# Kernel tuning notes

Measured on AMD Instinct MI355X. Metric: run time of the kernel, lower is better.

The kernel has to match this reference:

```python
import jax, jax.numpy as jnp
import numpy as np

T, H = 4096, 2048

def _glorot(key, shape):
    return jax.random.uniform(key, shape, minval=-1.0, maxval=1.0) * jnp.sqrt(2.0 / sum(shape))

def setup_inputs() -> dict:
    key = jax.random.key(0)
    k_x, k_a, k_b = jax.random.split(key, 3)
    x_seq = jax.random.normal(k_x, (T, H), dtype=jnp.float32)
    a_diag = _glorot(k_a, (H,)).astype(jnp.float32)        # (H,)
    b_mat = _glorot(k_b, (H, H)).astype(jnp.float32)       # (H, H)
    return {"x_seq": x_seq, "a_diag": a_diag, "b_mat": b_mat}

def _power_kernel(a_diag, length):
    # kernel[h, k] = a_diag[h] ** k for k in [0, length).
    # Computed via cumprod (identical math to jnp.power with integer exponents,
    # but well-defined for negative a_diag and differentiable).
    h = a_diag.shape[0]
    ones = jnp.ones((h, 1), dtype=a_diag.dtype)
    pows = jnp.cumprod(jnp.broadcast_to(a_diag[:, None], (h, length - 1)), axis=1)
    return jnp.concatenate([ones, pows], axis=1)[:, None, :]  # (H, 1, T)

def reference(x_seq, a_diag, b_mat):
    seq_len, hidden_size = x_seq.shape
    s = b_mat.T @ x_seq.T                                  # (H, T)
    s_padded = jnp.pad(s, ((0, 0), (seq_len - 1, 0)))[None, :, :]  # (1, H, 2T-1)
    kernel = _power_kernel(a_diag, seq_len)                # (H, 1, T)
    kernel_flipped = jnp.flip(kernel, axis=-1)
    conv_out = jax.lax.conv_general_dilated(
        s_padded, kernel_flipped,
        window_strides=(1,), padding="VALID",
        dimension_numbers=("NCT", "OIT", "NCT"),
        feature_group_count=hidden_size,
    )                                                      # (1, H, T)
    return conv_out[0].T                                   # (T, H)
```

## Files before the change

### kernel.cpp

```cpp
#include <hip/hip_runtime.h>
#include <cstdint>
#include <cstddef>

typedef short bf16x8 __attribute__((ext_vector_type(8)));
typedef float f32x4 __attribute__((ext_vector_type(4)));

__device__ __forceinline__ unsigned short f2bf(float f) {
    union { float f; uint32_t u; } v; v.f = f;
    uint32_t r = v.u + 0x7FFFu + ((v.u >> 16) & 1u);
    return (unsigned short)(r >> 16);
}

__device__ __forceinline__ float bf2f(unsigned short u) {
    union { uint32_t u; float f; } v; v.u = (uint32_t)u << 16;
    return v.f;
}


__global__ void prep_kernel(const float* __restrict__ X,
                            unsigned short* __restrict__ Xbf, int n4,
                            const float* __restrict__ B,
                            unsigned short* __restrict__ Bt, int H,
                            int castBlocks) {
    if ((int)blockIdx.x < castBlocks) {
        int i = blockIdx.x * 256 + threadIdx.x;
        if (i < n4) {
            float4 v = ((const float4*)X)[i];
            ushort4 o;
            o.x = f2bf(v.x); o.y = f2bf(v.y); o.z = f2bf(v.z); o.w = f2bf(v.w);
            ((ushort4*)Xbf)[i] = o;
        }
        return;
    }
    __shared__ float tile[32][33];
    int tb = blockIdx.x - castBlocks;
    int tilesPerRow = H / 32;
    int bx = (tb % tilesPerRow) * 32;
    int by = (tb / tilesPerRow) * 32;
    int tx = threadIdx.x & 31, ty = threadIdx.x >> 5;
#pragma unroll
    for (int i = 0; i < 32; i += 8)
        tile[ty + i][tx] = B[(size_t)(by + ty + i) * H + bx + tx];
    __syncthreads();
#pragma unroll
    for (int i = 0; i < 32; i += 8)
        Bt[(size_t)(bx + ty + i) * H + by + tx] = f2bf(tile[tx][ty + i]);
}


__global__ __launch_bounds__(256, 2) void gemm_scan_fused(
    const unsigned short* __restrict__ A,
    const unsigned short* __restrict__ Bt,
    const float* __restrict__ Ad,
    float* __restrict__ out,
    int M, int N, int K, int gridMt)
{
    extern __shared__ char smem[];

    const int tid  = threadIdx.x;
    const int wave = tid >> 6;
    const int lane = tid & 63;

    int b = blockIdx.x;
    int mt, nt;
    if ((gridMt & 7) == 0) {
        int x = b & 7, g = b >> 3;
        int mPerX = gridMt >> 3;
        mt = x * mPerX + (g % mPerX);
        nt = g / mPerX;
    } else {
        mt = b % gridMt;
        nt = b / gridMt;
    }
    const int m0 = mt * 128;
    const int n0 = nt * 128;

    const int wm = wave >> 1;
    const int wn = wave & 1;
    const int srow = lane >> 3;
    const int scol = ((lane & 7) ^ srow) * 8;
    const int quad = lane >> 4;
    const int l16  = lane & 15;
    const int s7   = l16 & 7;
    const int koff0 = (quad ^ s7) * 16;
    const int koff1 = ((quad + 4) ^ s7) * 16;
    const int hi8  = l16 >> 3;

    f32x4 acc[4][4];
#pragma unroll
    for (int i = 0; i < 4; ++i)
#pragma unroll
        for (int j = 0; j < 4; ++j)
            acc[i][j] = (f32x4){0.f, 0.f, 0.f, 0.f};
    f32x4 wacc[2];
    wacc[0] = (f32x4){0.f, 0.f, 0.f, 0.f};
    wacc[1] = (f32x4){0.f, 0.f, 0.f, 0.f};

    const int NT = K >> 6;

    auto STAGE = [&](int bufoff, int k0) {
#pragma unroll
        for (int i = 0; i < 9; ++i) {
            const int t = wave + i * 4;
            if (t < 33) {
                const unsigned short* g;
                if (t < 17) {
                    int gr = m0 - 8 + t * 8 + srow;
                    if (gr < 0) gr = 0;
                    g = A + (size_t)gr * K + (k0 + scol);
                } else {
                    const int gr = n0 + (t - 17) * 8 + srow;
                    g = Bt + (size_t)gr * K + (k0 + scol);
                }
                __builtin_amdgcn_global_load_lds(
                    (const __attribute__((address_space(1))) void*)g,
                    (__attribute__((address_space(3))) void*)
                        (smem + bufoff + t * 1024 + lane * 16),
                    16, 0, 0);
            }
        }
    };

    STAGE(0, 0);
    __syncthreads();

    for (int t = 0; t < NT; ++t) {
        const int cur = (t & 1) * 33792;
        if (t + 1 < NT)
            STAGE((~t & 1) * 33792, (t + 1) * 64);

        const char* base = smem + cur;
#pragma unroll
        for (int kk = 0; kk < 2; ++kk) {
            const int co = kk ? koff1 : koff0;
            bf16x8 af[4], bfr[4], aw, bw0, bw1;
            aw = *(const bf16x8*)(base + hi8 * 1024 + s7 * 128 + co);
#pragma unroll
            for (int im = 0; im < 4; ++im)
                af[im] = *(const bf16x8*)(base +
                    (1 + wm * 8 + im * 2 + hi8) * 1024 + s7 * 128 + co);
#pragma unroll
            for (int in = 0; in < 4; ++in)
                bfr[in] = *(const bf16x8*)(base +
                    (17 + wn * 8 + in * 2 + hi8) * 1024 + s7 * 128 + co);
            bw0 = *(const bf16x8*)(base +
                    (17 + (wave * 2 + 0) * 2 + hi8) * 1024 + s7 * 128 + co);
            bw1 = *(const bf16x8*)(base +
                    (17 + (wave * 2 + 1) * 2 + hi8) * 1024 + s7 * 128 + co);
            wacc[0] = __builtin_amdgcn_mfma_f32_16x16x32_bf16(aw, bw0, wacc[0], 0, 0, 0);
            wacc[1] = __builtin_amdgcn_mfma_f32_16x16x32_bf16(aw, bw1, wacc[1], 0, 0, 0);
#pragma unroll
            for (int im = 0; im < 4; ++im)
#pragma unroll
                for (int in = 0; in < 4; ++in)
                    acc[im][in] = __builtin_amdgcn_mfma_f32_16x16x32_bf16(
                        af[im], bfr[in], acc[im][in], 0, 0, 0);
        }
        __syncthreads();
    }

    unsigned short* Sl = (unsigned short*)smem;
#pragma unroll
    for (int im = 0; im < 4; ++im)
#pragma unroll
        for (int in = 0; in < 4; ++in) {
            const int col = wn * 64 + in * 16 + l16;
#pragma unroll
            for (int r = 0; r < 4; ++r) {
                const int row = 8 + wm * 64 + im * 16 + quad * 4 + r;
                Sl[row * 132 + col] = f2bf(acc[im][in][r]);
            }
        }
    if (quad < 2) {
#pragma unroll
        for (int j = 0; j < 2; ++j) {
            const int wcol = (wave * 2 + j) * 16 + l16;
#pragma unroll
            for (int r = 0; r < 4; ++r)
                Sl[(quad * 4 + r) * 132 + wcol] = f2bf(wacc[j][r]);
        }
    }
    __syncthreads();

    const int c = tid & 127;
    const int q = tid >> 7;
    const float aa = Ad[n0 + c];
    float y = 0.f;
    if (mt != 0 || q != 0) {
#pragma unroll
        for (int i = 0; i < 8; ++i)
            y = fmaf(aa, y, bf2f(Sl[(q * 64 + i) * 132 + c]));
    }
    const size_t ob = (size_t)(m0 + q * 64) * N + n0 + c;
    const unsigned short* Sr = Sl + (8 + q * 64) * 132 + c;
    for (int t = 0; t < 64; ++t) {
        y = fmaf(aa, y, bf2f(Sr[t * 132]));
        out[ob + (size_t)t * N] = y;
    }
}


__global__ __launch_bounds__(256, 2) void gemm_sk_bf16out(
    const unsigned short* __restrict__ A,
    const unsigned short* __restrict__ Bt,
    unsigned short* __restrict__ S0, unsigned short* __restrict__ S1,
    int M, int N, int K, int gridM, int gridN)
{
    __shared__ __attribute__((aligned(16))) unsigned short sA[256 * 64];
    __shared__ __attribute__((aligned(16))) unsigned short sB[128 * 64];

    const int tid  = threadIdx.x;
    const int wave = tid >> 6;
    const int lane = tid & 63;

    int b = blockIdx.x;
    int mt, nt, kt;
    if ((gridM & 7) == 0) {
        int x = b & 7, g = b >> 3;
        int mPerX = gridM >> 3;
        int ml = g % mPerX, g2 = g / mPerX;
        nt = g2 % gridN;
        kt = g2 / gridN;
        mt = x * mPerX + ml;
    } else {
        mt = b % gridM;
        nt = (b / gridM) % gridN;
        kt = b / (gridM * gridN);
    }
    const int m0 = mt * 256;
    const int n0 = nt * 128;
    const int ksize = K / 2;
    const int kbase = kt * ksize;

    const int srow = lane >> 3;
    const int scol = ((lane & 7) ^ srow) * 8;

    const int quad = lane >> 4;
    const int l16  = lane & 15;
    const int wm = wave >> 1;
    const int wn = wave & 1;
    const int s7 = l16 & 7;
    const int c0 = (quad ^ s7) * 16;
    const int c1 = ((quad + 4) ^ s7) * 16;

    f32x4 acc[8][4];
#pragma unroll
    for (int i = 0; i < 8; ++i)
#pragma unroll
        for (int j = 0; j < 4; ++j)
            acc[i][j] = (f32x4){0.f, 0.f, 0.f, 0.f};

    const unsigned short* Ab = A  + (size_t)m0 * K;
    const unsigned short* Bb = Bt + (size_t)n0 * K;

    const int rA = (wm * 16 + (l16 >> 3)) * 1024 + s7 * 128;
    const int rB = (wn * 8  + (l16 >> 3)) * 1024 + s7 * 128;

    for (int k0 = kbase; k0 < kbase + ksize; k0 += 64) {
#pragma unroll
        for (int i = 0; i < 8; ++i) {
            const int t = wave * 8 + i;
            const unsigned short* ga = Ab + (size_t)(t * 8 + srow) * K + (k0 + scol);
            __builtin_amdgcn_global_load_lds(
                (const __attribute__((address_space(1))) void*)ga,
                (__attribute__((address_space(3))) void*)(sA + t * 512),
                16, 0, 0);
        }
#pragma unroll
        for (int i = 0; i < 4; ++i) {
            const int t = wave * 4 + i;
            const unsigned short* gb = Bb + (size_t)(t * 8 + srow) * K + (k0 + scol);
            __builtin_amdgcn_global_load_lds(
                (const __attribute__((address_space(1))) void*)gb,
                (__attribute__((address_space(3))) void*)(sB + t * 512),
                16, 0, 0);
        }
        __syncthreads();

#pragma unroll
        for (int kk = 0; kk < 2; ++kk) {
            const int co = kk ? c1 : c0;
            bf16x8 af[8], bfr[4];
#pragma unroll
            for (int im = 0; im < 8; ++im)
                af[im] = *(const bf16x8*)((const char*)sA + rA + im * 2048 + co);
#pragma unroll
            for (int in = 0; in < 4; ++in)
                bfr[in] = *(const bf16x8*)((const char*)sB + rB + in * 2048 + co);
#pragma unroll
            for (int im = 0; im < 8; ++im)
#pragma unroll
                for (int in = 0; in < 4; ++in)
                    acc[im][in] = __builtin_amdgcn_mfma_f32_16x16x32_bf16(
                        af[im], bfr[in], acc[im][in], 0, 0, 0);
        }
        __syncthreads();
    }

    unsigned short* __restrict__ S = (kt == 0) ? S0 : S1;
#pragma unroll
    for (int im = 0; im < 8; ++im) {
#pragma unroll
        for (int in = 0; in < 4; ++in) {
            int col = n0 + wn * 64 + in * 16 + l16;
#pragma unroll
            for (int r = 0; r < 4; ++r) {
                int row = m0 + wm * 128 + im * 16 + quad * 4 + r;
                S[(size_t)row * N + col] = f2bf(acc[im][in][r]);
            }
        }
    }
}


__device__ __forceinline__ void stage_tile128(
    const unsigned short* __restrict__ Ab, const unsigned short* __restrict__ Bb,
    unsigned short* sAp, unsigned short* sBp,
    int wave, int srow, int scol, int k0, int K)
{
#pragma unroll
    for (int i = 0; i < 4; ++i) {
        const int t = wave * 4 + i;
        const unsigned short* ga = Ab + (size_t)(t * 8 + srow) * K + (k0 + scol);
        __builtin_amdgcn_global_load_lds(
            (const __attribute__((address_space(1))) void*)ga,
            (__attribute__((address_space(3))) void*)(sAp + t * 512),
            16, 0, 0);
        const unsigned short* gb = Bb + (size_t)(t * 8 + srow) * K + (k0 + scol);
        __builtin_amdgcn_global_load_lds(
            (const __attribute__((address_space(1))) void*)gb,
            (__attribute__((address_space(3))) void*)(sBp + t * 512),
            16, 0, 0);
    }
}

__global__ __launch_bounds__(256, 4) void gemm_f32out(
    const unsigned short* __restrict__ A,
    const unsigned short* __restrict__ Bt,
    float* __restrict__ C, int M, int N, int K, int gridM)
{
    __shared__ __attribute__((aligned(16))) unsigned short sA[128 * 64];
    __shared__ __attribute__((aligned(16))) unsigned short sB[128 * 64];

    const int tid  = threadIdx.x;
    const int wave = tid >> 6;
    const int lane = tid & 63;

    int b = blockIdx.x;
    int mt, nt;
    if ((gridM & 7) == 0) {
        int x = b & 7, g = b >> 3;
        int mPerX = gridM >> 3;
        mt = x * mPerX + (g % mPerX);
        nt = g / mPerX;
    } else {
        mt = b % gridM;
        nt = b / gridM;
    }
    const int m0 = mt * 128;
    const int n0 = nt * 128;

    const int srow = lane >> 3;
    const int scol = ((lane & 7) ^ srow) * 8;
    const int quad = lane >> 4;
    const int l16  = lane & 15;
    const int wm = wave >> 1;
    const int wn = wave & 1;
    const int s7 = l16 & 7;
    const int rbaseA = (wm * 8 + (l16 >> 3)) * 1024 + s7 * 128;
    const int rbaseB = (wn * 8 + (l16 >> 3)) * 1024 + s7 * 128;
    const int coff0 = (quad ^ s7) * 16;
    const int coff1 = ((quad + 4) ^ s7) * 16;

    f32x4 acc[4][4];
#pragma unroll
    for (int i = 0; i < 4; ++i)
#pragma unroll
        for (int j = 0; j < 4; ++j)
            acc[i][j] = (f32x4){0.f, 0.f, 0.f, 0.f};

    const unsigned short* Ab = A  + (size_t)m0 * K;
    const unsigned short* Bb = Bt + (size_t)n0 * K;

    for (int k0 = 0; k0 < K; k0 += 64) {
        stage_tile128(Ab, Bb, sA, sB, wave, srow, scol, k0, K);
        __syncthreads();
        bf16x8 af[2][4], bfr[2][4];
#pragma unroll
        for (int t = 0; t < 4; ++t) {
            const char* pa = (const char*)sA + rbaseA + t * 2048;
            af[0][t]  = *(const bf16x8*)(pa + coff0);
            af[1][t]  = *(const bf16x8*)(pa + coff1);
            const char* pb = (const char*)sB + rbaseB + t * 2048;
            bfr[0][t] = *(const bf16x8*)(pb + coff0);
            bfr[1][t] = *(const bf16x8*)(pb + coff1);
        }
#pragma unroll
        for (int kk = 0; kk < 2; ++kk)
#pragma unroll
            for (int im = 0; im < 4; ++im)
#pragma unroll
                for (int in = 0; in < 4; ++in)
                    acc[im][in] = __builtin_amdgcn_mfma_f32_16x16x32_bf16(
                        af[kk][im], bfr[kk][in], acc[im][in], 0, 0, 0);
        __syncthreads();
    }

#pragma unroll
    for (int im = 0; im < 4; ++im)
#pragma unroll
        for (int in = 0; in < 4; ++in) {
            int col = n0 + wn * 64 + in * 16 + l16;
#pragma unroll
            for (int r = 0; r < 4; ++r) {
                int row = m0 + wm * 64 + im * 16 + quad * 4 + r;
                C[(size_t)row * N + col] = acc[im][in][r];
            }
        }
}


__global__ void scan_splitk_bf16(const unsigned short* __restrict__ S0,
                                 const unsigned short* __restrict__ S1,
                                 const float* __restrict__ a_diag,
                                 float* __restrict__ out,
                                 int H2, int chunk) {
    int tid = blockIdx.x * blockDim.x + threadIdx.x;
    int hp = tid % H2, c = tid / H2;
    float2 av = ((const float2*)a_diag)[hp];
    const ushort2* S0v = (const ushort2*)S0;
    const ushort2* S1v = (const ushort2*)S1;
    float2* outv = (float2*)out;

    float y0 = 0.f, y1 = 0.f;
    if (c > 0) {
        size_t r0 = (size_t)c * chunk - 8;
#pragma unroll
        for (int i = 0; i < 8; ++i) {
            size_t idx = (r0 + i) * H2 + hp;
            ushort2 u = S0v[idx], w = S1v[idx];
            y0 = fmaf(av.x, y0, bf2f(u.x) + bf2f(w.x));
            y1 = fmaf(av.y, y1, bf2f(u.y) + bf2f(w.y));
        }
    }
    size_t idx = (size_t)c * chunk * H2 + hp;
    ushort2 u = S0v[idx], w = S1v[idx];
    for (int t = 0; t < chunk - 1; ++t) {
        size_t idx2 = idx + H2;
        ushort2 un = S0v[idx2], wn = S1v[idx2];
        y0 = fmaf(av.x, y0, bf2f(u.x) + bf2f(w.x));
        y1 = fmaf(av.y, y1, bf2f(u.y) + bf2f(w.y));
        outv[idx] = make_float2(y0, y1);
        u = un; w = wn; idx = idx2;
    }
    y0 = fmaf(av.x, y0, bf2f(u.x) + bf2f(w.x));
    y1 = fmaf(av.y, y1, bf2f(u.y) + bf2f(w.y));
    outv[idx] = make_float2(y0, y1);
}


__global__ void scan_init_kernel(const float* __restrict__ S,
                                 const float* __restrict__ a_diag,
                                 float* __restrict__ yinit,
                                 int H, int chunk, int W) {
    int tid = blockIdx.x * blockDim.x + threadIdx.x;
    int h = tid % H, c = tid / H;
    float a = a_diag[h];
    float y = 0.f;
    if (c > 0) {
        int t0 = c * chunk;
        for (int t = t0 - W; t < t0; ++t)
            y = fmaf(a, y, S[(size_t)t * H + h]);
    }
    yinit[(size_t)c * H + h] = y;
}

__global__ void scan_run_kernel(const float* __restrict__ yinit,
                                const float* __restrict__ a_diag,
                                float* __restrict__ out,
                                int H, int chunk) {
    int tid = blockIdx.x * blockDim.x + threadIdx.x;
    int h = tid % H, c = tid / H;
    float a = a_diag[h];
    float y = yinit[(size_t)c * H + h];
    size_t base = (size_t)c * chunk * H + h;
    float s = out[base];
#pragma unroll 4
    for (int t = 0; t < chunk - 1; ++t) {
        float snext = out[base + (size_t)(t + 1) * H];
        y = fmaf(a, y, s);
        out[base + (size_t)t * H] = y;
        s = snext;
    }
    y = fmaf(a, y, s);
    out[base + (size_t)(chunk - 1) * H] = y;
}


__global__ void gemm_fallback(const float* __restrict__ X, const float* __restrict__ B,
                              float* __restrict__ C, int M, int N, int K) {
    __shared__ float sA[16][17];
    __shared__ float sB[16][17];
    int tx = threadIdx.x, ty = threadIdx.y;
    int row = blockIdx.y * 16 + ty, col = blockIdx.x * 16 + tx;
    float acc = 0.f;
    for (int k0 = 0; k0 < K; k0 += 16) {
        sA[ty][tx] = (row < M && k0 + tx < K) ? X[(size_t)row * K + k0 + tx] : 0.f;
        sB[ty][tx] = (k0 + ty < K && col < N) ? B[(size_t)(k0 + ty) * N + col] : 0.f;
        __syncthreads();
#pragma unroll
        for (int kk = 0; kk < 16; ++kk) acc += sA[ty][kk] * sB[kk][tx];
        __syncthreads();
    }
    if (row < M && col < N) C[(size_t)row * N + col] = acc;
}

__global__ void scan_serial(float* __restrict__ out, const float* __restrict__ a_diag,
                            int T, int H) {
    int h = blockIdx.x * blockDim.x + threadIdx.x;
    if (h >= H) return;
    float a = a_diag[h], y = 0.f;
    for (int t = 0; t < T; ++t) {
        y = fmaf(a, y, out[(size_t)t * H + h]);
        out[(size_t)t * H + h] = y;
    }
}


extern "C" void kernel_launch(void* const* d_in, const int* in_sizes, int n_in,
                              void* d_out, int out_size, void* d_ws, size_t ws_size,
                              hipStream_t stream) {
    const float* x = (const float*)d_in[0];
    const float* a = (const float*)d_in[1];
    const float* b = (const float*)d_in[2];
    float* out = (float*)d_out;

    const int H = in_sizes[1];
    const int T = in_sizes[0] / H;
    const int M = T, N = H, K = H;

    const int CHUNK = 16, W = 12;

    size_t xbf_elems = (size_t)M * K;
    size_t bt_elems  = (size_t)N * K;
    size_t MN = (size_t)M * N;
    int nchunks = (T % CHUNK == 0) ? T / CHUNK : 0;

    size_t need_fused = (xbf_elems + bt_elems) * 2 + 256;
    size_t need_sk  = (xbf_elems + bt_elems + 2 * MN) * 2 + 256;
    size_t need_mid = xbf_elems * 2 + bt_elems * 2 + 256;

    bool shape_ok = (M % 128 == 0) && (N % 128 == 0) && (K % 128 == 0) &&
                    (H % 32 == 0) && nchunks > 0 && ((xbf_elems % 4) == 0) &&
                    (((size_t)nchunks * H) % 256 == 0);
    int gridMf = M / 128;
    int gridM  = (M % 256 == 0) ? M / 256 : 0;
    int gridN  = N / 128;

    int n4 = (int)(xbf_elems / 4);
    int castBlocks = (n4 + 255) / 256;
    int transBlocks = (H % 32 == 0) ? (H / 32) * (H / 32) : 0;

    int H2 = H / 2;
    size_t nth2 = (size_t)nchunks * H2;

    bool fused_ok = (M % 128 == 0) && (N % 128 == 0) && (K % 64 == 0) &&
                    (K >= 128) && (H % 32 == 0) && ((xbf_elems % 4) == 0) &&
                    ws_size >= need_fused;

    if (fused_ok) {
        unsigned short* Xbf = (unsigned short*)d_ws;
        unsigned short* Bt  = Xbf + xbf_elems;

        static bool gfattr = false;
        if (!gfattr) {
            (void)hipFuncSetAttribute((const void*)gemm_scan_fused,
                                      hipFuncAttributeMaxDynamicSharedMemorySize,
                                      67584);
            gfattr = true;
        }

        prep_kernel<<<castBlocks + transBlocks, 256, 0, stream>>>(
            x, Xbf, n4, b, Bt, H, castBlocks);

        gemm_scan_fused<<<(M / 128) * (N / 128), 256, 67584, stream>>>(
            Xbf, Bt, a, out, M, N, K, M / 128);
    } else if (shape_ok && gridM > 0 && (gridM % 8 == 0) && (H % 4 == 0) &&
               (nth2 % 256 == 0) && ws_size >= need_sk) {
        unsigned short* Xbf = (unsigned short*)d_ws;
        unsigned short* Bt  = Xbf + xbf_elems;
        unsigned short* S0  = Bt + bt_elems;
        unsigned short* S1  = S0 + MN;

        prep_kernel<<<castBlocks + transBlocks, 256, 0, stream>>>(
            x, Xbf, n4, b, Bt, H, castBlocks);

        gemm_sk_bf16out<<<gridM * gridN * 2, 256, 0, stream>>>(
            Xbf, Bt, S0, S1, M, N, K, gridM, gridN);

        scan_splitk_bf16<<<(int)(nth2 / 256), 256, 0, stream>>>(
            S0, S1, a, out, H2, CHUNK);
    } else if (shape_ok && ws_size >= need_mid &&
               ((size_t)nchunks * H * 4 <= xbf_elems * 2)) {
        unsigned short* Xbf = (unsigned short*)d_ws;
        unsigned short* Bt  = Xbf + xbf_elems;
        float* yinit = (float*)d_ws;

        prep_kernel<<<castBlocks + transBlocks, 256, 0, stream>>>(
            x, Xbf, n4, b, Bt, H, castBlocks);

        gemm_f32out<<<gridMf * gridN, 256, 0, stream>>>(
            Xbf, Bt, out, M, N, K, gridMf);

        int nth = nchunks * H;
        scan_init_kernel<<<nth / 256, 256, 0, stream>>>(out, a, yinit, H, CHUNK, W);
        scan_run_kernel<<<nth / 256, 256, 0, stream>>>(yinit, a, out, H, CHUNK);
    } else {
        dim3 tb(16, 16), tg((N + 15) / 16, (M + 15) / 16);
        gemm_fallback<<<tg, tb, 0, stream>>>(x, b, out, M, N, K);
        scan_serial<<<(H + 255) / 256, 256, 0, stream>>>(out, a, T, H);
    }
}
```

Before: 137.3 us.

## Enlarge fused GEMM-scan tile to 256x128 rows per block

Doubles the M tile of the fused GEMM+scan kernel from 128 to 256 rows, so each wave computes 8x4 MFMA tiles and the 8-row halo overhead is amortized over twice the rows. The halo MFMA work is moved to the wm==0 waves and reuses the B fragments already loaded. LDS grows to about 100 KB and occupancy drops to one block per CU. The grid halves to 256 blocks, and the sequential scan per thread doubles to 128 steps.

Result: slower. 147.8 us (+7.7%).

```diff
diff --git a/kernel.cpp b/kernel.cpp
--- a/kernel.cpp
+++ b/kernel.cpp
@@ -48,7 +48,7 @@
 }
 
 
-__global__ __launch_bounds__(256, 2) void gemm_scan_fused(
+__global__ __launch_bounds__(256, 1) void gemm_scan_fused(
     const unsigned short* __restrict__ A,
     const unsigned short* __restrict__ Bt,
     const float* __restrict__ Ad,
@@ -72,7 +72,7 @@
         mt = b % gridMt;
         nt = b / gridMt;
     }
-    const int m0 = mt * 128;
+    const int m0 = mt * 256;
     const int n0 = nt * 128;
 
     const int wm = wave >> 1;
@@ -86,30 +86,34 @@
     const int koff1 = ((quad + 4) ^ s7) * 16;
     const int hi8  = l16 >> 3;
 
-    f32x4 acc[4][4];
-#pragma unroll
-    for (int i = 0; i < 4; ++i)
+    const int rA = (1 + wm * 16 + hi8) * 1024 + s7 * 128;
+    const int rB = (33 + wn * 8 + hi8) * 1024 + s7 * 128;
+
+    f32x4 acc[8][4];
+#pragma unroll
+    for (int i = 0; i < 8; ++i)
 #pragma unroll
         for (int j = 0; j < 4; ++j)
             acc[i][j] = (f32x4){0.f, 0.f, 0.f, 0.f};
-    f32x4 wacc[2];
-    wacc[0] = (f32x4){0.f, 0.f, 0.f, 0.f};
-    wacc[1] = (f32x4){0.f, 0.f, 0.f, 0.f};
+    f32x4 wacc[4];
+#pragma unroll
+    for (int j = 0; j < 4; ++j)
+        wacc[j] = (f32x4){0.f, 0.f, 0.f, 0.f};
 
     const int NT = K >> 6;
 
     auto STAGE = [&](int bufoff, int k0) {
 #pragma unroll
-        for (int i = 0; i < 9; ++i) {
+        for (int i = 0; i < 13; ++i) {
             const int t = wave + i * 4;
-            if (t < 33) {
+            if (t < 49) {
                 const unsigned short* g;
-                if (t < 17) {
+                if (t < 33) {
                     int gr = m0 - 8 + t * 8 + srow;
                     if (gr < 0) gr = 0;
                     g = A + (size_t)gr * K + (k0 + scol);
                 } else {
-                    const int gr = n0 + (t - 17) * 8 + srow;
+                    const int gr = n0 + (t - 33) * 8 + srow;
                     g = Bt + (size_t)gr * K + (k0 + scol);
                 }
                 __builtin_amdgcn_global_load_lds(
@@ -125,59 +129,57 @@
     __syncthreads();
 
     for (int t = 0; t < NT; ++t) {
-        const int cur = (t & 1) * 33792;
+        const int cur = (t & 1) * 50176;
         if (t + 1 < NT)
-            STAGE((~t & 1) * 33792, (t + 1) * 64);
+            STAGE((~t & 1) * 50176, (t + 1) * 64);
 
         const char* base = smem + cur;
 #pragma unroll
         for (int kk = 0; kk < 2; ++kk) {
             const int co = kk ? koff1 : koff0;
-            bf16x8 af[4], bfr[4], aw, bw0, bw1;
-            aw = *(const bf16x8*)(base + hi8 * 1024 + s7 * 128 + co);
-#pragma unroll
-            for (int im = 0; im < 4; ++im)
-                af[im] = *(const bf16x8*)(base +
-                    (1 + wm * 8 + im * 2 + hi8) * 1024 + s7 * 128 + co);
+            bf16x8 af[8], bfr[4];
+#pragma unroll
+            for (int im = 0; im < 8; ++im)
+                af[im] = *(const bf16x8*)(base + rA + im * 2048 + co);
 #pragma unroll
             for (int in = 0; in < 4; ++in)
-                bfr[in] = *(const bf16x8*)(base +
-                    (17 + wn * 8 + in * 2 + hi8) * 1024 + s7 * 128 + co);
-            bw0 = *(const bf16x8*)(base +
-                    (17 + (wave * 2 + 0) * 2 + hi8) * 1024 + s7 * 128 + co);
-            bw1 = *(const bf16x8*)(base +
-                    (17 + (wave * 2 + 1) * 2 + hi8) * 1024 + s7 * 128 + co);
-            wacc[0] = __builtin_amdgcn_mfma_f32_16x16x32_bf16(aw, bw0, wacc[0], 0, 0, 0);
-            wacc[1] = __builtin_amdgcn_mfma_f32_16x16x32_bf16(aw, bw1, wacc[1], 0, 0, 0);
-#pragma unroll
-            for (int im = 0; im < 4; ++im)
+                bfr[in] = *(const bf16x8*)(base + rB + in * 2048 + co);
+#pragma unroll
+            for (int im = 0; im < 8; ++im)
 #pragma unroll
                 for (int in = 0; in < 4; ++in)
                     acc[im][in] = __builtin_amdgcn_mfma_f32_16x16x32_bf16(
                         af[im], bfr[in], acc[im][in], 0, 0, 0);
+            if (wm == 0) {
+                bf16x8 aw = *(const bf16x8*)(base + hi8 * 1024 + s7 * 128 + co);
+#pragma unroll
+                for (int in = 0; in < 4; ++in)
+                    wacc[in] = __builtin_amdgcn_mfma_f32_16x16x32_bf16(
+                        aw, bfr[in], wacc[in], 0, 0, 0);
+            }
         }
         __syncthreads();
     }
 
     unsigned short* Sl = (unsigned short*)smem;
 #pragma unroll
-    for (int im = 0; im < 4; ++im)
+    for (int im = 0; im < 8; ++im)
 #pragma unroll
         for (int in = 0; in < 4; ++in) {
             const int col = wn * 64 + in * 16 + l16;
 #pragma unroll
             for (int r = 0; r < 4; ++r) {
-                const int row = 8 + wm * 64 + im * 16 + quad * 4 + r;
+                const int row = 8 + wm * 128 + im * 16 + quad * 4 + r;
                 Sl[row * 132 + col] = f2bf(acc[im][in][r]);
             }
         }
-    if (quad < 2) {
-#pragma unroll
-        for (int j = 0; j < 2; ++j) {
-            const int wcol = (wave * 2 + j) * 16 + l16;
+    if (wm == 0 && quad < 2) {
+#pragma unroll
+        for (int in = 0; in < 4; ++in) {
+            const int col = wn * 64 + in * 16 + l16;
 #pragma unroll
             for (int r = 0; r < 4; ++r)
-                Sl[(quad * 4 + r) * 132 + wcol] = f2bf(wacc[j][r]);
+                Sl[(quad * 4 + r) * 132 + col] = f2bf(wacc[in][r]);
         }
     }
     __syncthreads();
@@ -189,11 +191,11 @@
     if (mt != 0 || q != 0) {
 #pragma unroll
         for (int i = 0; i < 8; ++i)
-            y = fmaf(aa, y, bf2f(Sl[(q * 64 + i) * 132 + c]));
-    }
-    const size_t ob = (size_t)(m0 + q * 64) * N + n0 + c;
-    const unsigned short* Sr = Sl + (8 + q * 64) * 132 + c;
-    for (int t = 0; t < 64; ++t) {
+            y = fmaf(aa, y, bf2f(Sl[(q * 128 + i) * 132 + c]));
+    }
+    const size_t ob = (size_t)(m0 + q * 128) * N + n0 + c;
+    const unsigned short* Sr = Sl + (8 + q * 128) * 132 + c;
+    for (int t = 0; t < 128; ++t) {
         y = fmaf(aa, y, bf2f(Sr[t * 132]));
         out[ob + (size_t)t * N] = y;
     }
@@ -564,7 +566,7 @@
     int H2 = H / 2;
     size_t nth2 = (size_t)nchunks * H2;
 
-    bool fused_ok = (M % 128 == 0) && (N % 128 == 0) && (K % 64 == 0) &&
+    bool fused_ok = (M % 256 == 0) && (N % 128 == 0) && (K % 64 == 0) &&
                     (K >= 128) && (H % 32 == 0) && ((xbf_elems % 4) == 0) &&
                     ws_size >= need_fused;
 
@@ -576,15 +578,15 @@
         if (!gfattr) {
             (void)hipFuncSetAttribute((const void*)gemm_scan_fused,
                                       hipFuncAttributeMaxDynamicSharedMemorySize,
-                                      67584);
+                                      100352);
             gfattr = true;
         }
 
         prep_kernel<<<castBlocks + transBlocks, 256, 0, stream>>>(
             x, Xbf, n4, b, Bt, H, castBlocks);
 
-        gemm_scan_fused<<<(M / 128) * (N / 128), 256, 67584, stream>>>(
-            Xbf, Bt, a, out, M, N, K, M / 128);
+        gemm_scan_fused<<<(M / 256) * (N / 128), 256, 100352, stream>>>(
+            Xbf, Bt, a, out, M, N, K, M / 256);
     } else if (shape_ok && gridM > 0 && (gridM % 8 == 0) && (H % 4 == 0) &&
                (nth2 % 256 == 0) && ws_size >= need_sk) {
         unsigned short* Xbf = (unsigned short*)d_ws;
```
